# Performance work log

Measured on AMD Instinct MI355X. Metric: run time of the kernel, lower is better.

## Reference

```python
import jax, jax.numpy as jnp
import numpy as np

B, N, IN_F, H, DEG, L = 4096, 64, 32, 128, 8, 2
E = N * DEG
ALPHA = 0.2  # LeakyReLU slope
EPS = 1e-5   # LayerNorm eps


def setup_inputs() -> dict:
    key = jax.random.key(0)
    ks = jax.random.split(key, 16)
    # ring graph: node i -> (i+k) mod N for k=1..DEG (unique edges, every node has out-edges)
    src = jnp.repeat(jnp.arange(N, dtype=jnp.int32), DEG)
    dst = ((src + jnp.tile(jnp.arange(1, DEG + 1, dtype=jnp.int32), N)) % N).astype(jnp.int32)
    edge_index = jnp.stack([src, dst])  # (2, E)
    Hh = H // 2
    inp = {
        "x": jax.random.normal(ks[0], (B, IN_F), jnp.float32),
        "station_idx": jax.random.randint(ks[1], (B,), 0, N, jnp.int32),
        "edge_index": edge_index,
        "edge_weight": jax.random.uniform(ks[2], (E,), jnp.float32, 0.1, 1.0),
        "Wp": jax.random.normal(ks[3], (IN_F, H), jnp.float32) / np.sqrt(IN_F),
        "bp": jnp.zeros((H,), jnp.float32),
        "emb": jax.random.normal(ks[4], (N, Hh), jnp.float32) * 0.02,
        "gat_W": jax.random.normal(ks[5], (L, H, H), jnp.float32) / np.sqrt(H),
        "gat_a": jax.random.normal(ks[6], (L, 2 * H), jnp.float32) * 0.1,
        "W1": jax.random.normal(ks[7], (H + Hh, H), jnp.float32) / np.sqrt(H + Hh),
        "b1": jnp.zeros((H,), jnp.float32),
        "g1": jnp.ones((H,), jnp.float32),
        "be1": jnp.zeros((H,), jnp.float32),
        "W2": jax.random.normal(ks[8], (H, Hh), jnp.float32) / np.sqrt(H),
        "b2": jnp.zeros((Hh,), jnp.float32),
        "g2": jnp.ones((Hh,), jnp.float32),
        "be2": jnp.zeros((Hh,), jnp.float32),
        "Wo": jax.random.normal(ks[9], (Hh, 1), jnp.float32) / np.sqrt(Hh),
        "bo": jnp.zeros((1,), jnp.float32),
    }
    return inp


def _layernorm(v, g, b):
    m = v.mean(-1, keepdims=True)
    var = ((v - m) ** 2).mean(-1, keepdims=True)
    return (v - m) / jnp.sqrt(var + EPS) * g + b


def _gat(h, W, a, src, dst, edge_weight):
    # h: (B, N, H); W: (H, H); a: (2H,)
    Wh = jnp.einsum('bnf,fg->bng', h, W)
    s_src = Wh @ a[:H]   # (B, N)
    s_dst = Wh @ a[H:]   # (B, N)
    e = jax.nn.leaky_relu(s_src[:, src] + s_dst[:, dst], ALPHA)  # (B, E)
    e = e * edge_weight[None, :]
    att = jnp.zeros((h.shape[0], N, N), h.dtype).at[:, src, dst].set(e)
    mask = att == 0  # faithfully reproduces the torch zero-mask trick
    att = jnp.where(mask, -jnp.inf, att)
    att = jax.nn.softmax(att, axis=2)
    att = jnp.where(mask, 0.0, att)
    # dropout is identity at inference
    return jax.nn.elu(jnp.einsum('bnm,bmf->bnf', att, Wh))


def reference(x, station_idx, edge_index, edge_weight, Wp, bp, emb, gat_W, gat_a,
              W1, b1, g1, be1, W2, b2, g2, be2, Wo, bo):
    src, dst = edge_index[0], edge_index[1]
    h0 = x @ Wp + bp                               # (B, H)
    h = jnp.broadcast_to(h0[:, None, :], (x.shape[0], N, H))
    for i in range(L):
        h = h + _gat(h, gat_W[i], gat_a[i], src, dst, edge_weight)
    h_node = h[jnp.arange(x.shape[0]), station_idx]  # (B, H)
    s = emb[station_idx]                              # (B, H//2)
    z = jnp.concatenate([h_node, s], axis=-1)
    z = jax.nn.relu(_layernorm(z @ W1 + b1, g1, be1))
    z = jax.nn.relu(_layernorm(z @ W2 + b2, g2, be2))
    return (z @ Wo + bo).squeeze(-1)                  # (B,)
```

## Files before the change

### kernel.cpp

```cpp
#include <hip/hip_runtime.h>
#include <math.h>

namespace {

constexpr int INF = 32;
constexpr int H   = 128;
constexpr int HH  = 64;
constexpr int ZD  = 192;
constexpr int SPB = 8;
constexpr float LNEPS = 1e-5f;

__device__ __forceinline__ float elu1(float v) {
    return v > 0.f ? v : (__expf(v) - 1.f);
}

template<int DK, int LDW, int NS>
__device__ __forceinline__ void gemm_part(const float* __restrict__ Wcol,
                                          const float* __restrict__ act,
                                          float* __restrict__ t)
{
    if constexpr (DK == 8) {
        float w[8];
#pragma unroll
        for (int r = 0; r < 8; ++r) w[r] = Wcol[r * LDW];
#pragma unroll
        for (int rr = 0; rr < 8; rr += 4) {
#pragma unroll
            for (int s = 0; s < NS; ++s) {
                const float4 hv = *reinterpret_cast<const float4*>(act + s * ZD + rr);
                t[s] += hv.x * w[rr + 0] + hv.y * w[rr + 1]
                      + hv.z * w[rr + 2] + hv.w * w[rr + 3];
            }
        }
    } else {
        constexpr int NC = DK / 8;
        static_assert((NC & 1) == 0, "even chunk count");
        float wa[8], wb[8];
#pragma unroll
        for (int r = 0; r < 8; ++r) wa[r] = Wcol[r * LDW];
#pragma unroll
        for (int c = 0; c < NC; c += 2) {
#pragma unroll
            for (int r = 0; r < 8; ++r) wb[r] = Wcol[((c + 1) * 8 + r) * LDW];
#pragma unroll
            for (int rr = 0; rr < 8; rr += 4) {
#pragma unroll
                for (int s = 0; s < NS; ++s) {
                    const float4 hv = *reinterpret_cast<const float4*>(act + s * ZD + c * 8 + rr);
                    t[s] += hv.x * wa[rr + 0] + hv.y * wa[rr + 1]
                          + hv.z * wa[rr + 2] + hv.w * wa[rr + 3];
                }
            }
            if (c + 2 < NC) {
#pragma unroll
                for (int r = 0; r < 8; ++r) wa[r] = Wcol[((c + 2) * 8 + r) * LDW];
            }
#pragma unroll
            for (int rr = 0; rr < 8; rr += 4) {
#pragma unroll
                for (int s = 0; s < NS; ++s) {
                    const float4 hv = *reinterpret_cast<const float4*>(act + s * ZD + (c + 1) * 8 + rr);
                    t[s] += hv.x * wb[rr + 0] + hv.y * wb[rr + 1]
                          + hv.z * wb[rr + 2] + hv.w * wb[rr + 3];
                }
            }
        }
    }
}

__global__ __launch_bounds__(512, 4) void fused_sthgat(
    const float* __restrict__ x, const int* __restrict__ sid,
    const float* __restrict__ Wp, const float* __restrict__ bp,
    const float* __restrict__ emb, const float* __restrict__ gatW,
    const float* __restrict__ W1, const float* __restrict__ b1,
    const float* __restrict__ g1, const float* __restrict__ be1,
    const float* __restrict__ W2, const float* __restrict__ b2,
    const float* __restrict__ g2, const float* __restrict__ be2,
    const float* __restrict__ Wo, const float* __restrict__ bo,
    float* __restrict__ out)
{
    __shared__ __align__(16) float P2[4 * SPB * H];
    __shared__ __align__(16) float buf0[SPB * ZD];
    __shared__ __align__(16) float buf1[SPB * ZD];
    __shared__ float Rbuf[4][2][2][2];

    const int tid  = threadIdx.x;
    const int lane = tid & 63;
    const int wid  = tid >> 6;
    const int kq   = tid >> 7;
    const int g    = tid & 127;
    const int sbase = blockIdx.x * SPB;

    if (tid < SPB * INF) {
        buf0[(tid >> 5) * ZD + (tid & 31)] = x[(size_t)sbase * INF + tid];
    }
    __syncthreads();

    {
        float t[SPB] = {0,0,0,0,0,0,0,0};
        gemm_part<8, H, SPB>(Wp + (kq * 8) * H + g, buf0 + kq * 8, t);
#pragma unroll
        for (int s = 0; s < SPB; ++s) P2[kq * (SPB * H) + s * H + g] = t[s];
        __syncthreads();
        const float bpv = bp[g];
#pragma unroll
        for (int e = 0; e < 2; ++e) {
            const int s = kq * 2 + e;
            const float v = P2[0 * (SPB * H) + s * H + g] + P2[1 * (SPB * H) + s * H + g]
                          + P2[2 * (SPB * H) + s * H + g] + P2[3 * (SPB * H) + s * H + g] + bpv;
            buf1[s * ZD + g] = v;
        }
        __syncthreads();
    }

    {
        float t[SPB] = {0,0,0,0,0,0,0,0};
        gemm_part<32, H, SPB>(gatW + (kq * 32) * H + g, buf1 + kq * 32, t);
#pragma unroll
        for (int s = 0; s < SPB; ++s) P2[kq * (SPB * H) + s * H + g] = t[s];
        __syncthreads();
#pragma unroll
        for (int e = 0; e < 2; ++e) {
            const int s = kq * 2 + e;
            const float v = P2[0 * (SPB * H) + s * H + g] + P2[1 * (SPB * H) + s * H + g]
                          + P2[2 * (SPB * H) + s * H + g] + P2[3 * (SPB * H) + s * H + g];
            buf0[s * ZD + g] = buf1[s * ZD + g] + elu1(v);
        }
        __syncthreads();
    }

    {
        float t[SPB] = {0,0,0,0,0,0,0,0};
        gemm_part<32, H, SPB>(gatW + H * H + (kq * 32) * H + g, buf0 + kq * 32, t);
#pragma unroll
        for (int s = 0; s < SPB; ++s) P2[kq * (SPB * H) + s * H + g] = t[s];
        __syncthreads();
#pragma unroll
        for (int e = 0; e < 2; ++e) {
            const int s = kq * 2 + e;
            const float v = P2[0 * (SPB * H) + s * H + g] + P2[1 * (SPB * H) + s * H + g]
                          + P2[2 * (SPB * H) + s * H + g] + P2[3 * (SPB * H) + s * H + g];
            buf1[s * ZD + g] = buf0[s * ZD + g] + elu1(v);
        }
        {
            const int st = sid[sbase + wid];
            buf1[wid * ZD + H + lane] = emb[st * HH + lane];
        }
        __syncthreads();
    }

    {
        float t[SPB] = {0,0,0,0,0,0,0,0};
        gemm_part<48, H, SPB>(W1 + (kq * 48) * H + g, buf1 + kq * 48, t);
#pragma unroll
        for (int s = 0; s < SPB; ++s) P2[kq * (SPB * H) + s * H + g] = t[s];
        __syncthreads();
        const float b1v = b1[g];
        float u[2];
#pragma unroll
        for (int e = 0; e < 2; ++e) {
            const int s = kq * 2 + e;
            u[e] = P2[0 * (SPB * H) + s * H + g] + P2[1 * (SPB * H) + s * H + g]
                 + P2[2 * (SPB * H) + s * H + g] + P2[3 * (SPB * H) + s * H + g] + b1v;
        }
        float su[2], sq[2];
#pragma unroll
        for (int e = 0; e < 2; ++e) { su[e] = u[e]; sq[e] = u[e] * u[e]; }
#pragma unroll
        for (int off = 32; off >= 1; off >>= 1) {
#pragma unroll
            for (int e = 0; e < 2; ++e) {
                su[e] += __shfl_xor(su[e], off, 64);
                sq[e] += __shfl_xor(sq[e], off, 64);
            }
        }
        if (lane == 0) {
            const int h = g >> 6;
#pragma unroll
            for (int e = 0; e < 2; ++e) {
                Rbuf[kq][h][e][0] = su[e];
                Rbuf[kq][h][e][1] = sq[e];
            }
        }
        __syncthreads();
        const float g1v = g1[g], be1v = be1[g];
#pragma unroll
        for (int e = 0; e < 2; ++e) {
            const int s = kq * 2 + e;
            const float tot = Rbuf[kq][0][e][0] + Rbuf[kq][1][e][0];
            const float tq  = Rbuf[kq][0][e][1] + Rbuf[kq][1][e][1];
            const float m   = tot * (1.f / H);
            const float var = tq * (1.f / H) - m * m;
            const float rs  = rsqrtf(var + LNEPS);
            buf0[s * ZD + g] = fmaxf((u[e] - m) * rs * g1v + be1v, 0.f);
        }
        __syncthreads();
    }

    {
        const int c = lane;
        float t[SPB] = {0,0,0,0,0,0,0,0};
        gemm_part<16, HH, SPB>(W2 + (wid * 16) * HH + c, buf0 + wid * 16, t);
#pragma unroll
        for (int s = 0; s < SPB; ++s) P2[wid * (SPB * HH) + s * HH + c] = t[s];
        __syncthreads();
        float v = b2[c];
#pragma unroll
        for (int k = 0; k < 8; ++k) v += P2[k * (SPB * HH) + wid * HH + c];
        float su = v, sq = v * v;
#pragma unroll
        for (int off = 32; off >= 1; off >>= 1) {
            su += __shfl_xor(su, off, 64);
            sq += __shfl_xor(sq, off, 64);
        }
        const float m   = su * (1.f / HH);
        const float var = sq * (1.f / HH) - m * m;
        const float rs  = rsqrtf(var + LNEPS);
        const float z2  = fmaxf((v - m) * rs * g2[c] + be2[c], 0.f);
        float po = z2 * Wo[c];
#pragma unroll
        for (int off = 32; off >= 1; off >>= 1) po += __shfl_xor(po, off, 64);
        if (lane == 0) out[sbase + wid] = po + bo[0];
    }
}

}

extern "C" void kernel_launch(void* const* d_in, const int* in_sizes, int n_in,
                              void* d_out, int out_size, void* d_ws, size_t ws_size,
                              hipStream_t stream)
{
    const float* x    = (const float*)d_in[0];
    const int*   sid  = (const int*)d_in[1];
    const float* Wp   = (const float*)d_in[4];
    const float* bp   = (const float*)d_in[5];
    const float* emb  = (const float*)d_in[6];
    const float* gatW = (const float*)d_in[7];
    const float* W1   = (const float*)d_in[9];
    const float* b1   = (const float*)d_in[10];
    const float* g1   = (const float*)d_in[11];
    const float* be1  = (const float*)d_in[12];
    const float* W2   = (const float*)d_in[13];
    const float* b2   = (const float*)d_in[14];
    const float* g2   = (const float*)d_in[15];
    const float* be2  = (const float*)d_in[16];
    const float* Wo   = (const float*)d_in[17];
    const float* bo   = (const float*)d_in[18];
    float* out = (float*)d_out;

    dim3 grid(4096 / SPB);
    dim3 block(512);
    hipLaunchKernelGGL(fused_sthgat, grid, block, 0, stream,
                       x, sid, Wp, bp, emb, gatW, W1, b1, g1, be1,
                       W2, b2, g2, be2, Wo, bo, out);
}
```

Before: 104.7 us.

## Halve samples per block and compute two output columns per thread

```diff
diff --git a/kernel.cpp b/kernel.cpp
--- a/kernel.cpp
+++ b/kernel.cpp
@@ -7,68 +7,87 @@
 constexpr int H   = 128;
 constexpr int HH  = 64;
 constexpr int ZD  = 192;
-constexpr int SPB = 8;
+constexpr int SPB = 4;
 constexpr float LNEPS = 1e-5f;
 
 __device__ __forceinline__ float elu1(float v) {
     return v > 0.f ? v : (__expf(v) - 1.f);
 }
 
-template<int DK, int LDW, int NS>
-__device__ __forceinline__ void gemm_part(const float* __restrict__ Wcol,
-                                          const float* __restrict__ act,
-                                          float* __restrict__ t)
+template<int DKq, int LDW, int NCOL>
+__device__ __forceinline__ void gemm2(const float* __restrict__ W0,
+                                      const float* __restrict__ act,
+                                      float (&t)[SPB][NCOL])
 {
-    if constexpr (DK == 8) {
-        float w[8];
-#pragma unroll
-        for (int r = 0; r < 8; ++r) w[r] = Wcol[r * LDW];
+    if constexpr (DKq == 8) {
+        float w[8 * NCOL];
+#pragma unroll
+        for (int r = 0; r < 8; ++r)
+#pragma unroll
+            for (int c = 0; c < NCOL; ++c) w[r * NCOL + c] = W0[r * LDW + c * 64];
 #pragma unroll
         for (int rr = 0; rr < 8; rr += 4) {
 #pragma unroll
-            for (int s = 0; s < NS; ++s) {
+            for (int s = 0; s < SPB; ++s) {
                 const float4 hv = *reinterpret_cast<const float4*>(act + s * ZD + rr);
-                t[s] += hv.x * w[rr + 0] + hv.y * w[rr + 1]
-                      + hv.z * w[rr + 2] + hv.w * w[rr + 3];
+#pragma unroll
+                for (int c = 0; c < NCOL; ++c) {
+                    t[s][c] += hv.x * w[(rr + 0) * NCOL + c] + hv.y * w[(rr + 1) * NCOL + c]
+                             + hv.z * w[(rr + 2) * NCOL + c] + hv.w * w[(rr + 3) * NCOL + c];
+                }
             }
         }
     } else {
-        constexpr int NC = DK / 8;
-        static_assert((NC & 1) == 0, "even chunk count");
-        float wa[8], wb[8];
-#pragma unroll
-        for (int r = 0; r < 8; ++r) wa[r] = Wcol[r * LDW];
-#pragma unroll
-        for (int c = 0; c < NC; c += 2) {
-#pragma unroll
-            for (int r = 0; r < 8; ++r) wb[r] = Wcol[((c + 1) * 8 + r) * LDW];
+        constexpr int NCH = DKq / 8;
+        static_assert((NCH & 1) == 0, "even chunk count");
+        float wa[8 * NCOL], wb[8 * NCOL];
+#pragma unroll
+        for (int r = 0; r < 8; ++r)
+#pragma unroll
+            for (int c = 0; c < NCOL; ++c) wa[r * NCOL + c] = W0[r * LDW + c * 64];
+#pragma unroll
+        for (int ch = 0; ch < NCH; ch += 2) {
+#pragma unroll
+            for (int r = 0; r < 8; ++r)
+#pragma unroll
+                for (int c = 0; c < NCOL; ++c)
+                    wb[r * NCOL + c] = W0[((ch + 1) * 8 + r) * LDW + c * 64];
 #pragma unroll
             for (int rr = 0; rr < 8; rr += 4) {
 #pragma unroll
-                for (int s = 0; s < NS; ++s) {
-                    const float4 hv = *reinterpret_cast<const float4*>(act + s * ZD + c * 8 + rr);
-                    t[s] += hv.x * wa[rr + 0] + hv.y * wa[rr + 1]
-                          + hv.z * wa[rr + 2] + hv.w * wa[rr + 3];
+                for (int s = 0; s < SPB; ++s) {
+                    const float4 hv = *reinterpret_cast<const float4*>(act + s * ZD + ch * 8 + rr);
+#pragma unroll
+                    for (int c = 0; c < NCOL; ++c) {
+                        t[s][c] += hv.x * wa[(rr + 0) * NCOL + c] + hv.y * wa[(rr + 1) * NCOL + c]
+                                 + hv.z * wa[(rr + 2) * NCOL + c] + hv.w * wa[(rr + 3) * NCOL + c];
+                    }
                 }
             }
-            if (c + 2 < NC) {
-#pragma unroll
-                for (int r = 0; r < 8; ++r) wa[r] = Wcol[((c + 2) * 8 + r) * LDW];
+            if (ch + 2 < NCH) {
+#pragma unroll
+                for (int r = 0; r < 8; ++r)
+#pragma unroll
+                    for (int c = 0; c < NCOL; ++c)
+                        wa[r * NCOL + c] = W0[((ch + 2) * 8 + r) * LDW + c * 64];
             }
 #pragma unroll
             for (int rr = 0; rr < 8; rr += 4) {
 #pragma unroll
-                for (int s = 0; s < NS; ++s) {
-                    const float4 hv = *reinterpret_cast<const float4*>(act + s * ZD + (c + 1) * 8 + rr);
-                    t[s] += hv.x * wb[rr + 0] + hv.y * wb[rr + 1]
-                          + hv.z * wb[rr + 2] + hv.w * wb[rr + 3];
+                for (int s = 0; s < SPB; ++s) {
+                    const float4 hv = *reinterpret_cast<const float4*>(act + s * ZD + (ch + 1) * 8 + rr);
+#pragma unroll
+                    for (int c = 0; c < NCOL; ++c) {
+                        t[s][c] += hv.x * wb[(rr + 0) * NCOL + c] + hv.y * wb[(rr + 1) * NCOL + c]
+                                 + hv.z * wb[(rr + 2) * NCOL + c] + hv.w * wb[(rr + 3) * NCOL + c];
+                    }
                 }
             }
         }
     }
 }
 
-__global__ __launch_bounds__(512, 4) void fused_sthgat(
+__global__ __launch_bounds__(256, 4) void fused_sthgat(
     const float* __restrict__ x, const int* __restrict__ sid,
     const float* __restrict__ Wp, const float* __restrict__ bp,
     const float* __restrict__ emb, const float* __restrict__ gatW,
@@ -82,13 +101,12 @@
     __shared__ __align__(16) float P2[4 * SPB * H];
     __shared__ __align__(16) float buf0[SPB * ZD];
     __shared__ __align__(16) float buf1[SPB * ZD];
-    __shared__ float Rbuf[4][2][2][2];
 
     const int tid  = threadIdx.x;
     const int lane = tid & 63;
-    const int wid  = tid >> 6;
-    const int kq   = tid >> 7;
-    const int g    = tid & 127;
+    const int kq   = tid >> 6;
+    const int c    = tid & 63;
+    const int sw   = tid >> 6;
     const int sbase = blockIdx.x * SPB;
 
     if (tid < SPB * INF) {
@@ -97,116 +115,110 @@
     __syncthreads();
 
     {
-        float t[SPB] = {0,0,0,0,0,0,0,0};
-        gemm_part<8, H, SPB>(Wp + (kq * 8) * H + g, buf0 + kq * 8, t);
-#pragma unroll
-        for (int s = 0; s < SPB; ++s) P2[kq * (SPB * H) + s * H + g] = t[s];
-        __syncthreads();
-        const float bpv = bp[g];
-#pragma unroll
-        for (int e = 0; e < 2; ++e) {
-            const int s = kq * 2 + e;
-            const float v = P2[0 * (SPB * H) + s * H + g] + P2[1 * (SPB * H) + s * H + g]
-                          + P2[2 * (SPB * H) + s * H + g] + P2[3 * (SPB * H) + s * H + g] + bpv;
-            buf1[s * ZD + g] = v;
-        }
-        __syncthreads();
-    }
-
-    {
-        float t[SPB] = {0,0,0,0,0,0,0,0};
-        gemm_part<32, H, SPB>(gatW + (kq * 32) * H + g, buf1 + kq * 32, t);
-#pragma unroll
-        for (int s = 0; s < SPB; ++s) P2[kq * (SPB * H) + s * H + g] = t[s];
-        __syncthreads();
-#pragma unroll
-        for (int e = 0; e < 2; ++e) {
-            const int s = kq * 2 + e;
-            const float v = P2[0 * (SPB * H) + s * H + g] + P2[1 * (SPB * H) + s * H + g]
-                          + P2[2 * (SPB * H) + s * H + g] + P2[3 * (SPB * H) + s * H + g];
-            buf0[s * ZD + g] = buf1[s * ZD + g] + elu1(v);
-        }
-        __syncthreads();
-    }
-
-    {
-        float t[SPB] = {0,0,0,0,0,0,0,0};
-        gemm_part<32, H, SPB>(gatW + H * H + (kq * 32) * H + g, buf0 + kq * 32, t);
-#pragma unroll
-        for (int s = 0; s < SPB; ++s) P2[kq * (SPB * H) + s * H + g] = t[s];
-        __syncthreads();
-#pragma unroll
-        for (int e = 0; e < 2; ++e) {
-            const int s = kq * 2 + e;
-            const float v = P2[0 * (SPB * H) + s * H + g] + P2[1 * (SPB * H) + s * H + g]
-                          + P2[2 * (SPB * H) + s * H + g] + P2[3 * (SPB * H) + s * H + g];
-            buf1[s * ZD + g] = buf0[s * ZD + g] + elu1(v);
-        }
+        float t[SPB][2] = {};
+        gemm2<8, H, 2>(Wp + (kq * 8) * H + c, buf0 + kq * 8, t);
+#pragma unroll
+        for (int s = 0; s < SPB; ++s) {
+            P2[kq * (SPB * H) + s * H + c]      = t[s][0];
+            P2[kq * (SPB * H) + s * H + c + 64] = t[s][1];
+        }
+        __syncthreads();
+        float v0 = bp[c], v1 = bp[c + 64];
+#pragma unroll
+        for (int k = 0; k < 4; ++k) {
+            v0 += P2[k * (SPB * H) + sw * H + c];
+            v1 += P2[k * (SPB * H) + sw * H + c + 64];
+        }
+        buf1[sw * ZD + c]      = v0;
+        buf1[sw * ZD + c + 64] = v1;
+        __syncthreads();
+    }
+
+    {
+        float t[SPB][2] = {};
+        gemm2<32, H, 2>(gatW + (kq * 32) * H + c, buf1 + kq * 32, t);
+#pragma unroll
+        for (int s = 0; s < SPB; ++s) {
+            P2[kq * (SPB * H) + s * H + c]      = t[s][0];
+            P2[kq * (SPB * H) + s * H + c + 64] = t[s][1];
+        }
+        __syncthreads();
+        float v0 = 0.f, v1 = 0.f;
+#pragma unroll
+        for (int k = 0; k < 4; ++k) {
+            v0 += P2[k * (SPB * H) + sw * H + c];
+            v1 += P2[k * (SPB * H) + sw * H + c + 64];
+        }
+        buf0[sw * ZD + c]      = buf1[sw * ZD + c]      + elu1(v0);
+        buf0[sw * ZD + c + 64] = buf1[sw * ZD + c + 64] + elu1(v1);
+        __syncthreads();
+    }
+
+    {
+        float t[SPB][2] = {};
+        gemm2<32, H, 2>(gatW + H * H + (kq * 32) * H + c, buf0 + kq * 32, t);
+#pragma unroll
+        for (int s = 0; s < SPB; ++s) {
+            P2[kq * (SPB * H) + s * H + c]      = t[s][0];
+            P2[kq * (SPB * H) + s * H + c + 64] = t[s][1];
+        }
+        __syncthreads();
+        float v0 = 0.f, v1 = 0.f;
+#pragma unroll
+        for (int k = 0; k < 4; ++k) {
+            v0 += P2[k * (SPB * H) + sw * H + c];
+            v1 += P2[k * (SPB * H) + sw * H + c + 64];
+        }
+        buf1[sw * ZD + c]      = buf0[sw * ZD + c]      + elu1(v0);
+        buf1[sw * ZD + c + 64] = buf0[sw * ZD + c + 64] + elu1(v1);
         {
-            const int st = sid[sbase + wid];
-            buf1[wid * ZD + H + lane] = emb[st * HH + lane];
-        }
-        __syncthreads();
-    }
-
-    {
-        float t[SPB] = {0,0,0,0,0,0,0,0};
-        gemm_part<48, H, SPB>(W1 + (kq * 48) * H + g, buf1 + kq * 48, t);
-#pragma unroll
-        for (int s = 0; s < SPB; ++s) P2[kq * (SPB * H) + s * H + g] = t[s];
-        __syncthreads();
-        const float b1v = b1[g];
-        float u[2];
-#pragma unroll
-        for (int e = 0; e < 2; ++e) {
-            const int s = kq * 2 + e;
-            u[e] = P2[0 * (SPB * H) + s * H + g] + P2[1 * (SPB * H) + s * H + g]
-                 + P2[2 * (SPB * H) + s * H + g] + P2[3 * (SPB * H) + s * H + g] + b1v;
-        }
-        float su[2], sq[2];
-#pragma unroll
-        for (int e = 0; e < 2; ++e) { su[e] = u[e]; sq[e] = u[e] * u[e]; }
+            const int st = sid[sbase + sw];
+            buf1[sw * ZD + H + c] = emb[st * HH + c];
+        }
+        __syncthreads();
+    }
+
+    {
+        float t[SPB][2] = {};
+        gemm2<48, H, 2>(W1 + (kq * 48) * H + c, buf1 + kq * 48, t);
+#pragma unroll
+        for (int s = 0; s < SPB; ++s) {
+            P2[kq * (SPB * H) + s * H + c]      = t[s][0];
+            P2[kq * (SPB * H) + s * H + c + 64] = t[s][1];
+        }
+        __syncthreads();
+        float u0 = b1[c], u1 = b1[c + 64];
+#pragma unroll
+        for (int k = 0; k < 4; ++k) {
+            u0 += P2[k * (SPB * H) + sw * H + c];
+            u1 += P2[k * (SPB * H) + sw * H + c + 64];
+        }
+        float su = u0 + u1;
+        float sq = u0 * u0 + u1 * u1;
 #pragma unroll
         for (int off = 32; off >= 1; off >>= 1) {
-#pragma unroll
-            for (int e = 0; e < 2; ++e) {
-                su[e] += __shfl_xor(su[e], off, 64);
-                sq[e] += __shfl_xor(sq[e], off, 64);
-            }
-        }
-        if (lane == 0) {
-            const int h = g >> 6;
-#pragma unroll
-            for (int e = 0; e < 2; ++e) {
-                Rbuf[kq][h][e][0] = su[e];
-                Rbuf[kq][h][e][1] = sq[e];
-            }
-        }
-        __syncthreads();
-        const float g1v = g1[g], be1v = be1[g];
-#pragma unroll
-        for (int e = 0; e < 2; ++e) {
-            const int s = kq * 2 + e;
-            const float tot = Rbuf[kq][0][e][0] + Rbuf[kq][1][e][0];
-            const float tq  = Rbuf[kq][0][e][1] + Rbuf[kq][1][e][1];
-            const float m   = tot * (1.f / H);
-            const float var = tq * (1.f / H) - m * m;
-            const float rs  = rsqrtf(var + LNEPS);
-            buf0[s * ZD + g] = fmaxf((u[e] - m) * rs * g1v + be1v, 0.f);
-        }
-        __syncthreads();
-    }
-
-    {
-        const int c = lane;
-        float t[SPB] = {0,0,0,0,0,0,0,0};
-        gemm_part<16, HH, SPB>(W2 + (wid * 16) * HH + c, buf0 + wid * 16, t);
-#pragma unroll
-        for (int s = 0; s < SPB; ++s) P2[wid * (SPB * HH) + s * HH + c] = t[s];
+            su += __shfl_xor(su, off, 64);
+            sq += __shfl_xor(sq, off, 64);
+        }
+        const float m   = su * (1.f / H);
+        const float var = sq * (1.f / H) - m * m;
+        const float rs  = rsqrtf(var + LNEPS);
+        buf0[sw * ZD + c]      = fmaxf((u0 - m) * rs * g1[c]      + be1[c],      0.f);
+        buf0[sw * ZD + c + 64] = fmaxf((u1 - m) * rs * g1[c + 64] + be1[c + 64], 0.f);
+        __syncthreads();
+    }
+
+    {
+        float t[SPB][1] = {};
+        gemm2<32, HH, 1>(W2 + (kq * 32) * HH + c, buf0 + kq * 32, t);
+#pragma unroll
+        for (int s = 0; s < SPB; ++s) {
+            P2[kq * (SPB * HH) + s * HH + c] = t[s][0];
+        }
         __syncthreads();
         float v = b2[c];
 #pragma unroll
-        for (int k = 0; k < 8; ++k) v += P2[k * (SPB * HH) + wid * HH + c];
+        for (int k = 0; k < 4; ++k) v += P2[k * (SPB * HH) + sw * HH + c];
         float su = v, sq = v * v;
 #pragma unroll
         for (int off = 32; off >= 1; off >>= 1) {
@@ -220,7 +232,7 @@
         float po = z2 * Wo[c];
 #pragma unroll
         for (int off = 32; off >= 1; off >>= 1) po += __shfl_xor(po, off, 64);
-        if (lane == 0) out[sbase + wid] = po + bo[0];
+        if (lane == 0) out[sbase + sw] = po + bo[0];
     }
 }
 
@@ -249,7 +261,7 @@
     float* out = (float*)d_out;
 
     dim3 grid(4096 / SPB);
-    dim3 block(512);
+    dim3 block(256);
     hipLaunchKernelGGL(fused_sthgat, grid, block, 0, stream,
                        x, sid, Wp, bp, emb, gatW, W1, b1, g1, be1,
                        W2, b2, g2, be2, Wo, bo, out);
```

Result: no change. 104.8 us (+0.1%).
